# Kernel tuning notes

Measured on AMD Instinct MI355X. Metric: run time of the kernel, lower is better.

Reference implementation:

```python
import jax, jax.numpy as jnp
import numpy as np

B, T, C, H = 4, 4096, 1024, 64

def setup_inputs() -> dict:
    key = jax.random.key(0)
    kx, kq, kk, kv = jax.random.split(key, 4)
    x = jax.random.normal(kx, (B, T, C), dtype=jnp.float32)
    Wq = jax.random.normal(kq, (C, H), dtype=jnp.float32) * (C ** -0.5)
    Wk = jax.random.normal(kk, (C, H), dtype=jnp.float32) * (C ** -0.5)
    Wv = jax.random.normal(kv, (C, H), dtype=jnp.float32) * (C ** -0.5)
    return {"x": x, "Wq": Wq, "Wk": Wk, "Wv": Wv}

def reference(x, Wq, Wk, Wv):
    # single-head causal attention, dropout p=0 (eval)
    q = jnp.einsum('btc,ch->bth', x, Wq)  # [B,T,H]
    k = jnp.einsum('btc,ch->bth', x, Wk)
    v = jnp.einsum('btc,ch->bth', x, Wv)
    scale = k.shape[-1] ** -0.5
    scores = jnp.einsum('bth,bsh->bts', q, k) * scale  # [B,T,T]
    causal = jnp.tril(jnp.ones((q.shape[1], q.shape[1]), dtype=bool))
    scores = jnp.where(causal, scores, -jnp.inf)
    weights = jax.nn.softmax(scores, axis=-1)
    out = jnp.einsum('bts,bsh->bth', weights, v)  # [B,T,H]
    return out
```

## Files before the change

kernel.cpp:

```cpp
#include <hip/hip_runtime.h>


typedef short  s16x8 __attribute__((ext_vector_type(8)));
typedef float  f32x4 __attribute__((ext_vector_type(4)));
typedef unsigned u32x2 __attribute__((ext_vector_type(2)));

constexpr int B = 4, T = 4096, C = 1024, H = 64;
constexpr int M = B * T;
constexpr float LOG2E = 1.44269504088896340736f;
constexpr float QSCALE = 0.125f * LOG2E;
constexpr float MBASE  = 4.0f * LOG2E;

__device__ __forceinline__ unsigned short f2bf(float f) {
    union { float f; unsigned u; } v; v.f = f;
    unsigned r = v.u + 0x7fffu + ((v.u >> 16) & 1u);
    return (unsigned short)(r >> 16);
}

__device__ __forceinline__ unsigned cvt_pk_bf16(float lo, float hi) {
    unsigned r;
    asm("v_cvt_pk_bf16_f32 %0, %1, %2" : "=v"(r) : "v"(lo), "v"(hi));
    return r;
}

__device__ __forceinline__ float vexp2(float x) {
    float r;
    asm("v_exp_f32 %0, %1" : "=v"(r) : "v"(x));
    return r;
}

__device__ __forceinline__ void gl_lds16(const void* g, void* l) {
    __builtin_amdgcn_global_load_lds(
        (const __attribute__((address_space(1))) unsigned*)g,
        (__attribute__((address_space(3))) unsigned*)l, 16, 0, 0);
}

__global__ void prep_w(const float* __restrict__ Wq, const float* __restrict__ Wk,
                       const float* __restrict__ Wv, unsigned short* __restrict__ Wt) {
    const int n = blockIdx.x;
    const float* W = (n < 64) ? Wq : (n < 128 ? Wk : Wv);
    const int col = n & 63;
    for (int k = threadIdx.x; k < C; k += blockDim.x)
        Wt[(size_t)n * C + k] = f2bf(W[(size_t)k * H + col]);
}

__global__ __launch_bounds__(512) void qkv_proj(
    const float* __restrict__ x, const unsigned short* __restrict__ Wt,
    unsigned short* __restrict__ Q, unsigned short* __restrict__ K,
    unsigned short* __restrict__ VT) {
    __shared__ __align__(16) unsigned short ldsA[2][32 * 64];
    __shared__ __align__(16) unsigned short ldsB[2][192 * 64];

    const int t = threadIdx.x, lane = t & 63, w = t >> 6;
    const int i = lane & 15, g = lane >> 4;
    const int rowbase = blockIdx.x * 32;
    const int rw = w & 1, nw = w >> 1;

    const int arow = t >> 3, aslot = t & 7;
    const float* aga = x + (size_t)(rowbase + arow) * C + ((aslot ^ (arow & 7)) * 8);
    const int awoff = arow * 64 + aslot * 8;
    const bool astage = (t < 256);

    const int brow8 = lane >> 3, bslot = lane & 7;
    const unsigned short* bga[3];
    int bn0[3];
#pragma unroll
    for (int j = 0; j < 3; ++j) {
        bn0[j] = w * 24 + j * 8;
        bga[j] = Wt + (size_t)(bn0[j] + brow8) * C + ((bslot ^ brow8) * 8);
    }

    f32x4 acc[3];
#pragma unroll
    for (int n = 0; n < 3; ++n) acc[n] = (f32x4){0.f, 0.f, 0.f, 0.f};

    {
#pragma unroll
        for (int j = 0; j < 3; ++j)
            gl_lds16(bga[j], &ldsB[0][bn0[j] * 64]);
        if (astage) {
            f32x4 a0 = *(const f32x4*)(aga);
            f32x4 a1 = *(const f32x4*)(aga + 4);
            union { unsigned u[4]; s16x8 v; } av;
            av.u[0] = cvt_pk_bf16(a0[0], a0[1]);
            av.u[1] = cvt_pk_bf16(a0[2], a0[3]);
            av.u[2] = cvt_pk_bf16(a1[0], a1[1]);
            av.u[3] = cvt_pk_bf16(a1[2], a1[3]);
            *(s16x8*)&ldsA[0][awoff] = av.v;
        }
    }
    __syncthreads();

    for (int it = 0; it < 16; ++it) {
        const int cur = it & 1, nxt = cur ^ 1;
        const int kc = (it + 1) * 64;
        f32x4 a0, a1;
        const bool more = (it < 15);
        if (more) {
            if (astage) {
                a0 = *(const f32x4*)(aga + kc);
                a1 = *(const f32x4*)(aga + kc + 4);
            }
#pragma unroll
            for (int j = 0; j < 3; ++j)
                gl_lds16(bga[j] + kc, &ldsB[nxt][bn0[j] * 64]);
        }
#pragma unroll
        for (int kst = 0; kst < 2; ++kst) {
            const int c = kst * 4 + g;
            s16x8 a = *(const s16x8*)&ldsA[cur][(rw * 16 + i) * 64 + ((c ^ (i & 7)) * 8)];
#pragma unroll
            for (int nt = 0; nt < 3; ++nt) {
                int n = nw * 48 + nt * 16 + i;
                s16x8 b = *(const s16x8*)&ldsB[cur][n * 64 + ((c ^ (i & 7)) * 8)];
                acc[nt] = __builtin_amdgcn_mfma_f32_16x16x32_bf16(a, b, acc[nt], 0, 0, 0);
            }
        }
        if (more && astage) {
            union { unsigned u[4]; s16x8 v; } av;
            av.u[0] = cvt_pk_bf16(a0[0], a0[1]);
            av.u[1] = cvt_pk_bf16(a0[2], a0[3]);
            av.u[2] = cvt_pk_bf16(a1[0], a1[1]);
            av.u[3] = cvt_pk_bf16(a1[2], a1[3]);
            *(s16x8*)&ldsA[nxt][awoff] = av.v;
        }
        __syncthreads();
    }

#pragma unroll
    for (int nt = 0; nt < 3; ++nt) {
        const int base = nw * 48 + nt * 16;
        const int n = base + i;
        if (base >= 128) {
            const int h = n - 128;
            const int bb = rowbase >> 12, tb = rowbase & 4095;
            u32x2 pk;
            pk[0] = cvt_pk_bf16(acc[nt][0], acc[nt][1]);
            pk[1] = cvt_pk_bf16(acc[nt][2], acc[nt][3]);
            *(u32x2*)(VT + (size_t)(bb * H + h) * T + tb + g * 8 + rw * 4) = pk;
        } else if (base >= 64) {
#pragma unroll
            for (int r = 0; r < 4; ++r)
                K[(size_t)(rowbase + rw * 16 + g * 4 + r) * H + (n - 64)] = f2bf(acc[nt][r]);
        } else {
#pragma unroll
            for (int r = 0; r < 4; ++r)
                Q[(size_t)(rowbase + rw * 16 + g * 4 + r) * H + n] = f2bf(acc[nt][r] * QSCALE);
        }
    }
}

__global__ __launch_bounds__(256) void attn(
    const unsigned short* __restrict__ Qg, const unsigned short* __restrict__ Kg,
    const unsigned short* __restrict__ VTg,
    unsigned short* __restrict__ Opb, float* __restrict__ lpart) {
    __shared__ __align__(16) unsigned short ks[3][64 * 64];
    __shared__ __align__(16) unsigned short vs[3][64 * 64];

    const int t = threadIdx.x, lane = t & 63, w = t >> 6;
    const int bid = blockIdx.x;
    const int b = bid & 3;
    const int sp = (bid >> 2) & 7;
    const int qt = 31 - (bid >> 5);
    const int q0 = qt * 128;
    const int q0w = q0 + w * 32;
    const int i = lane & 15, g = lane >> 4, g4 = g * 4;
    const int nkv = 2 * qt + 2;
    const int nTiles = (sp < nkv) ? ((nkv - sp + 7) >> 3) : 0;

    const unsigned short* Kb = Kg  + (size_t)b * T * H;
    const unsigned short* Vb = VTg + (size_t)b * H * T;

    const int r8 = lane >> 3, sl = lane & 7, sx = sl ^ r8;

    const unsigned short* QrowA = Qg + (size_t)(b * T + q0w + i) * H;
    s16x8 bqa0 = *(const s16x8*)(QrowA + g * 8);
    s16x8 bqa1 = *(const s16x8*)(QrowA + 32 + g * 8);
    const unsigned short* QrowB = QrowA + 16 * H;
    s16x8 bqb0 = *(const s16x8*)(QrowB + g * 8);
    s16x8 bqb1 = *(const s16x8*)(QrowB + 32 + g * 8);

    const f32x4 minit = (f32x4){-MBASE, -MBASE, -MBASE, -MBASE};

    f32x4 oa[4], ob[4];
#pragma unroll
    for (int nt = 0; nt < 4; ++nt) {
        oa[nt] = (f32x4){0.f, 0.f, 0.f, 0.f};
        ob[nt] = (f32x4){0.f, 0.f, 0.f, 0.f};
    }
    float la = 0.f, lb = 0.f;

    if (nTiles > 0) {
        const int kv0 = sp * 64;
#pragma unroll
        for (int j = 0; j < 2; ++j) {
            const int row = (w + j * 4) * 8 + r8;
            gl_lds16(Kb + (size_t)(kv0 + row) * H + sx * 8, &ks[0][row * 64 + sl * 8]);
            gl_lds16(Vb + (size_t)row * T + kv0 + sx * 8,   &vs[0][row * 64 + sl * 8]);
        }
    }
    if (nTiles > 1) {
        const int kv1 = (sp + 8) * 64;
#pragma unroll
        for (int j = 0; j < 2; ++j) {
            const int row = (w + j * 4) * 8 + r8;
            gl_lds16(Kb + (size_t)(kv1 + row) * H + sx * 8, &ks[1][row * 64 + sl * 8]);
            gl_lds16(Vb + (size_t)row * T + kv1 + sx * 8,   &vs[1][row * 64 + sl * 8]);
        }
        asm volatile("s_waitcnt vmcnt(4)\n\ts_barrier" ::: "memory");
    } else {
        asm volatile("s_waitcnt vmcnt(0)\n\ts_barrier" ::: "memory");
    }

    for (int n = 0; n < nTiles; ++n) {
        const int tile = sp + n * 8;
        const int kv = tile * 64;
        const int cur = n % 3;
        const bool issue = (n + 2 < nTiles);

        if (issue) {
            const int nxt = (n + 2) % 3;
            const int kvn = kv + 1024;
#pragma unroll
            for (int j = 0; j < 2; ++j) {
                const int row = (w + j * 4) * 8 + r8;
                gl_lds16(Kb + (size_t)(kvn + row) * H + sx * 8, &ks[nxt][row * 64 + sl * 8]);
                gl_lds16(Vb + (size_t)row * T + kvn + sx * 8,   &vs[nxt][row * 64 + sl * 8]);
            }
        }

        if (kv <= q0w + 31) {
            s16x8 kb[8];
#pragma unroll
            for (int kst = 0; kst < 2; ++kst)
#pragma unroll
                for (int nt = 0; nt < 4; ++nt)
                    kb[kst * 4 + nt] = *(const s16x8*)
                        &ks[cur][(nt * 16 + i) * 64 + (((kst * 4 + g) ^ (i & 7)) * 8)];

            unsigned pa[8], pb2[8];

            {
                f32x4 s[4];
#pragma unroll
                for (int nt = 0; nt < 4; ++nt) {
                    s[nt] = __builtin_amdgcn_mfma_f32_16x16x32_bf16(kb[nt], bqa0, minit, 0, 0, 0);
                    s[nt] = __builtin_amdgcn_mfma_f32_16x16x32_bf16(kb[4 + nt], bqa1, s[nt], 0, 0, 0);
                }
                if (kv + 63 > q0w) {
                    const int thr = q0w + i - kv;
#pragma unroll
                    for (int nt = 0; nt < 4; ++nt)
#pragma unroll
                        for (int r = 0; r < 4; ++r)
                            if (nt * 16 + g4 + r > thr) s[nt][r] = -INFINITY;
                }
#pragma unroll
                for (int nt = 0; nt < 4; ++nt)
#pragma unroll
                    for (int r = 0; r < 4; ++r)
                        s[nt][r] = vexp2(s[nt][r]);
#pragma unroll
                for (int nt = 0; nt < 4; ++nt) {
                    pa[nt * 2]     = cvt_pk_bf16(s[nt][0], s[nt][1]);
                    pa[nt * 2 + 1] = cvt_pk_bf16(s[nt][2], s[nt][3]);
                }
                la += ((s[0][0] + s[0][1]) + (s[0][2] + s[0][3]))
                    + ((s[1][0] + s[1][1]) + (s[1][2] + s[1][3]))
                    + ((s[2][0] + s[2][1]) + (s[2][2] + s[2][3]))
                    + ((s[3][0] + s[3][1]) + (s[3][2] + s[3][3]));
            }

            {
                f32x4 s[4];
#pragma unroll
                for (int nt = 0; nt < 4; ++nt) {
                    s[nt] = __builtin_amdgcn_mfma_f32_16x16x32_bf16(kb[nt], bqb0, minit, 0, 0, 0);
                    s[nt] = __builtin_amdgcn_mfma_f32_16x16x32_bf16(kb[4 + nt], bqb1, s[nt], 0, 0, 0);
                }
                if (kv + 63 > q0w + 16) {
                    const int thr = q0w + 16 + i - kv;
#pragma unroll
                    for (int nt = 0; nt < 4; ++nt)
#pragma unroll
                        for (int r = 0; r < 4; ++r)
                            if (nt * 16 + g4 + r > thr) s[nt][r] = -INFINITY;
                }
#pragma unroll
                for (int nt = 0; nt < 4; ++nt)
#pragma unroll
                    for (int r = 0; r < 4; ++r)
                        s[nt][r] = vexp2(s[nt][r]);
#pragma unroll
                for (int nt = 0; nt < 4; ++nt) {
                    pb2[nt * 2]     = cvt_pk_bf16(s[nt][0], s[nt][1]);
                    pb2[nt * 2 + 1] = cvt_pk_bf16(s[nt][2], s[nt][3]);
                }
                lb += ((s[0][0] + s[0][1]) + (s[0][2] + s[0][3]))
                    + ((s[1][0] + s[1][1]) + (s[1][2] + s[1][3]))
                    + ((s[2][0] + s[2][1]) + (s[2][2] + s[2][3]))
                    + ((s[3][0] + s[3][1]) + (s[3][2] + s[3][3]));
            }

            s16x8 vb[8];
#pragma unroll
            for (int kst = 0; kst < 2; ++kst)
#pragma unroll
                for (int nt = 0; nt < 4; ++nt)
                    vb[kst * 4 + nt] = *(const s16x8*)
                        &vs[cur][(nt * 16 + i) * 64 + (((kst * 4 + g) ^ (i & 7)) * 8)];

#pragma unroll
            for (int kst = 0; kst < 2; ++kst) {
                union { unsigned u[4]; s16x8 v; } fa, fb;
                fa.u[0] = pa[4 * kst];      fa.u[1] = pa[4 * kst + 1];
                fa.u[2] = pa[4 * kst + 2];  fa.u[3] = pa[4 * kst + 3];
                fb.u[0] = pb2[4 * kst];     fb.u[1] = pb2[4 * kst + 1];
                fb.u[2] = pb2[4 * kst + 2]; fb.u[3] = pb2[4 * kst + 3];
#pragma unroll
                for (int nt = 0; nt < 4; ++nt) {
                    oa[nt] = __builtin_amdgcn_mfma_f32_16x16x32_bf16(vb[kst * 4 + nt], fa.v, oa[nt], 0, 0, 0);
                    ob[nt] = __builtin_amdgcn_mfma_f32_16x16x32_bf16(vb[kst * 4 + nt], fb.v, ob[nt], 0, 0, 0);
                }
            }
        }

        if (issue) asm volatile("s_waitcnt vmcnt(4)\n\ts_barrier" ::: "memory");
        else       asm volatile("s_waitcnt vmcnt(0)\n\ts_barrier" ::: "memory");
    }

    la += __shfl_xor(la, 16);  la += __shfl_xor(la, 32);
    lb += __shfl_xor(lb, 16);  lb += __shfl_xor(lb, 32);
    unsigned short* opA = Opb + ((size_t)bid * 128 + w * 32 + i) * 64;
    unsigned short* opB = opA + 16 * 64;
#pragma unroll
    for (int nt = 0; nt < 4; ++nt) {
        u32x2 pk;
        pk[0] = cvt_pk_bf16(oa[nt][0], oa[nt][1]);
        pk[1] = cvt_pk_bf16(oa[nt][2], oa[nt][3]);
        *(u32x2*)(opA + nt * 16 + g4) = pk;
        pk[0] = cvt_pk_bf16(ob[nt][0], ob[nt][1]);
        pk[1] = cvt_pk_bf16(ob[nt][2], ob[nt][3]);
        *(u32x2*)(opB + nt * 16 + g4) = pk;
    }
    if (g == 0) {
        lpart[(size_t)bid * 128 + w * 32 + i]      = la;
        lpart[(size_t)bid * 128 + w * 32 + 16 + i] = lb;
    }
}

__global__ __launch_bounds__(256) void merge8(
    const unsigned short* __restrict__ Opb, const float* __restrict__ lpart,
    float* __restrict__ out) {
    const int idx = blockIdx.x * 256 + threadIdx.x;
    const int row = idx >> 4, c4 = (idx & 15) * 4;
    const int b = row >> 12, q = row & 4095;
    const int qt = q >> 7, r = q & 127;
    const int qti = 31 - qt;

    float L = 0.f;
    f32x4 o = (f32x4){0.f, 0.f, 0.f, 0.f};
#pragma unroll
    for (int sp = 0; sp < 8; ++sp) {
        const int bidp = qti * 32 + sp * 4 + b;
        L += lpart[(size_t)bidp * 128 + r];
        union { unsigned long long d; unsigned short s[4]; } v;
        v.d = *(const unsigned long long*)&Opb[((size_t)bidp * 128 + r) * 64 + c4];
#pragma unroll
        for (int k = 0; k < 4; ++k) {
            union { unsigned u; float f; } cv;
            cv.u = (unsigned)v.s[k] << 16;
            o[k] += cv.f;
        }
    }
    const float inv = 1.0f / L;
    f32x4 res = (f32x4){o[0] * inv, o[1] * inv, o[2] * inv, o[3] * inv};
    *(f32x4*)&out[(size_t)row * 64 + c4] = res;
}

extern "C" void kernel_launch(void* const* d_in, const int* in_sizes, int n_in,
                              void* d_out, int out_size, void* d_ws, size_t ws_size,
                              hipStream_t stream) {
    (void)in_sizes; (void)n_in; (void)out_size; (void)ws_size;
    const float* x  = (const float*)d_in[0];
    const float* Wq = (const float*)d_in[1];
    const float* Wk = (const float*)d_in[2];
    const float* Wv = (const float*)d_in[3];
    float* out = (float*)d_out;

    char* ws = (char*)d_ws;
    unsigned short* Q  = (unsigned short*)(ws);
    unsigned short* K  = (unsigned short*)(ws + (size_t)1 * M * H * 2);
    unsigned short* VT = (unsigned short*)(ws + (size_t)3 * M * H * 2);
    unsigned short* Wt = (unsigned short*)(ws + (size_t)4 * M * H * 2);
    unsigned short* Opb = (unsigned short*)(ws + (size_t)4 * M * H * 2 + 512 * 1024);
    float* lpart = (float*)(ws + (size_t)4 * M * H * 2 + 512 * 1024
                            + (size_t)1024 * 128 * 64 * 2);

    prep_w<<<192, 256, 0, stream>>>(Wq, Wk, Wv, Wt);
    qkv_proj<<<M / 32, 512, 0, stream>>>(x, Wt, Q, K, VT);
    attn<<<1024, 256, 0, stream>>>(Q, K, VT, Opb, lpart);
    merge8<<<1024, 256, 0, stream>>>(Opb, lpart, out);
}
```

Baseline: 50.77 us.

## Compute softmax row sums via MFMA with ones and unroll triple-buffer loop

Replaces the per-lane VALU summation of exponentiated scores and the cross-lane shuffles with an extra MFMA against a vector of bf16 ones, so the row sum comes out of the matrix unit from the same bf16 probabilities used for PV. The tile loop is also unrolled by three with a templated body, making the LDS buffer index a compile-time constant instead of n%3. This trades VALU adds for extra MFMA issue slots and bigger code. The row sum now uses bf16-rounded probabilities, which is arguably more consistent with the numerator.

```diff
diff --git a/kernel.cpp b/kernel.cpp
--- a/kernel.cpp
+++ b/kernel.cpp
@@ -150,6 +150,123 @@
     }
 }
 
+template<int CUR>
+__device__ __forceinline__ void attn_tile(
+    int n, int nTiles, int sp, int q0w, int i, int g, int g4, int w,
+    int r8, int sl, int sx,
+    const unsigned short* Kb, const unsigned short* Vb,
+    unsigned short (&ks)[3][64 * 64], unsigned short (&vs)[3][64 * 64],
+    const s16x8& bqa0, const s16x8& bqa1, const s16x8& bqb0, const s16x8& bqb1,
+    const s16x8& ones, const f32x4& minit,
+    f32x4 (&oa)[4], f32x4 (&ob)[4], f32x4& al, f32x4& bl) {
+    constexpr int NXT = (CUR + 2) % 3;
+    const int kv = (sp + n * 8) * 64;
+    const bool issue = (n + 2 < nTiles);
+
+    if (issue) {
+        const int kvn = kv + 1024;
+#pragma unroll
+        for (int j = 0; j < 2; ++j) {
+            const int row = (w + j * 4) * 8 + r8;
+            gl_lds16(Kb + (size_t)(kvn + row) * H + sx * 8, &ks[NXT][row * 64 + sl * 8]);
+            gl_lds16(Vb + (size_t)row * T + kvn + sx * 8,   &vs[NXT][row * 64 + sl * 8]);
+        }
+    }
+
+    if (kv <= q0w + 31) {
+        s16x8 kb[8];
+#pragma unroll
+        for (int kst = 0; kst < 2; ++kst)
+#pragma unroll
+            for (int nt = 0; nt < 4; ++nt)
+                kb[kst * 4 + nt] = *(const s16x8*)
+                    &ks[CUR][(nt * 16 + i) * 64 + (((kst * 4 + g) ^ (i & 7)) * 8)];
+
+        unsigned pa[8], pb2[8];
+
+        {
+            f32x4 s[4];
+#pragma unroll
+            for (int nt = 0; nt < 4; ++nt) {
+                s[nt] = __builtin_amdgcn_mfma_f32_16x16x32_bf16(kb[nt], bqa0, minit, 0, 0, 0);
+                s[nt] = __builtin_amdgcn_mfma_f32_16x16x32_bf16(kb[4 + nt], bqa1, s[nt], 0, 0, 0);
+            }
+            if (kv + 63 > q0w) {
+                const int thr = q0w + i - kv;
+#pragma unroll
+                for (int nt = 0; nt < 4; ++nt)
+#pragma unroll
+                    for (int r = 0; r < 4; ++r)
+                        if (nt * 16 + g4 + r > thr) s[nt][r] = -INFINITY;
+            }
+#pragma unroll
+            for (int nt = 0; nt < 4; ++nt)
+#pragma unroll
+                for (int r = 0; r < 4; ++r)
+                    s[nt][r] = vexp2(s[nt][r]);
+#pragma unroll
+            for (int nt = 0; nt < 4; ++nt) {
+                pa[nt * 2]     = cvt_pk_bf16(s[nt][0], s[nt][1]);
+                pa[nt * 2 + 1] = cvt_pk_bf16(s[nt][2], s[nt][3]);
+            }
+        }
+
+        {
+            f32x4 s[4];
+#pragma unroll
+            for (int nt = 0; nt < 4; ++nt) {
+                s[nt] = __builtin_amdgcn_mfma_f32_16x16x32_bf16(kb[nt], bqb0, minit, 0, 0, 0);
+                s[nt] = __builtin_amdgcn_mfma_f32_16x16x32_bf16(kb[4 + nt], bqb1, s[nt], 0, 0, 0);
+            }
+            if (kv + 63 > q0w + 16) {
+                const int thr = q0w + 16 + i - kv;
+#pragma unroll
+                for (int nt = 0; nt < 4; ++nt)
+#pragma unroll
+                    for (int r = 0; r < 4; ++r)
+                        if (nt * 16 + g4 + r > thr) s[nt][r] = -INFINITY;
+            }
+#pragma unroll
+            for (int nt = 0; nt < 4; ++nt)
+#pragma unroll
+                for (int r = 0; r < 4; ++r)
+                    s[nt][r] = vexp2(s[nt][r]);
+#pragma unroll
+            for (int nt = 0; nt < 4; ++nt) {
+                pb2[nt * 2]     = cvt_pk_bf16(s[nt][0], s[nt][1]);
+                pb2[nt * 2 + 1] = cvt_pk_bf16(s[nt][2], s[nt][3]);
+            }
+        }
+
+        s16x8 vb[8];
+#pragma unroll
+        for (int kst = 0; kst < 2; ++kst)
+#pragma unroll
+            for (int nt = 0; nt < 4; ++nt)
+                vb[kst * 4 + nt] = *(const s16x8*)
+                    &vs[CUR][(nt * 16 + i) * 64 + (((kst * 4 + g) ^ (i & 7)) * 8)];
+
+#pragma unroll
+        for (int kst = 0; kst < 2; ++kst) {
+            union { unsigned u[4]; s16x8 v; } fa, fb;
+            fa.u[0] = pa[4 * kst];      fa.u[1] = pa[4 * kst + 1];
+            fa.u[2] = pa[4 * kst + 2];  fa.u[3] = pa[4 * kst + 3];
+            fb.u[0] = pb2[4 * kst];     fb.u[1] = pb2[4 * kst + 1];
+            fb.u[2] = pb2[4 * kst + 2]; fb.u[3] = pb2[4 * kst + 3];
+#pragma unroll
+            for (int nt = 0; nt < 4; ++nt) {
+                oa[nt] = __builtin_amdgcn_mfma_f32_16x16x32_bf16(vb[kst * 4 + nt], fa.v, oa[nt], 0, 0, 0);
+                ob[nt] = __builtin_amdgcn_mfma_f32_16x16x32_bf16(vb[kst * 4 + nt], fb.v, ob[nt], 0, 0, 0);
+            }
+            al = __builtin_amdgcn_mfma_f32_16x16x32_bf16(ones, fa.v, al, 0, 0, 0);
+            bl = __builtin_amdgcn_mfma_f32_16x16x32_bf16(ones, fb.v, bl, 0, 0, 0);
+        }
+    }
+
+    if (issue) asm volatile("s_waitcnt vmcnt(4)\n\ts_barrier" ::: "memory");
+    else       asm volatile("s_waitcnt vmcnt(0)\n\ts_barrier" ::: "memory");
+}
+
 __global__ __launch_bounds__(256) void attn(
     const unsigned short* __restrict__ Qg, const unsigned short* __restrict__ Kg,
     const unsigned short* __restrict__ VTg,
@@ -181,6 +298,9 @@
     s16x8 bqb1 = *(const s16x8*)(QrowB + 32 + g * 8);
 
     const f32x4 minit = (f32x4){-MBASE, -MBASE, -MBASE, -MBASE};
+    s16x8 ones;
+#pragma unroll
+    for (int j = 0; j < 8; ++j) ones[j] = (short)0x3F80;
 
     f32x4 oa[4], ob[4];
 #pragma unroll
@@ -188,7 +308,8 @@
         oa[nt] = (f32x4){0.f, 0.f, 0.f, 0.f};
         ob[nt] = (f32x4){0.f, 0.f, 0.f, 0.f};
     }
-    float la = 0.f, lb = 0.f;
+    f32x4 al = (f32x4){0.f, 0.f, 0.f, 0.f};
+    f32x4 bl = (f32x4){0.f, 0.f, 0.f, 0.f};
 
     if (nTiles > 0) {
         const int kv0 = sp * 64;
@@ -212,125 +333,21 @@
         asm volatile("s_waitcnt vmcnt(0)\n\ts_barrier" ::: "memory");
     }
 
-    for (int n = 0; n < nTiles; ++n) {
-        const int tile = sp + n * 8;
-        const int kv = tile * 64;
-        const int cur = n % 3;
-        const bool issue = (n + 2 < nTiles);
-
-        if (issue) {
-            const int nxt = (n + 2) % 3;
-            const int kvn = kv + 1024;
-#pragma unroll
-            for (int j = 0; j < 2; ++j) {
-                const int row = (w + j * 4) * 8 + r8;
-                gl_lds16(Kb + (size_t)(kvn + row) * H + sx * 8, &ks[nxt][row * 64 + sl * 8]);
-                gl_lds16(Vb + (size_t)row * T + kvn + sx * 8,   &vs[nxt][row * 64 + sl * 8]);
-            }
-        }
-
-        if (kv <= q0w + 31) {
-            s16x8 kb[8];
-#pragma unroll
-            for (int kst = 0; kst < 2; ++kst)
-#pragma unroll
-                for (int nt = 0; nt < 4; ++nt)
-                    kb[kst * 4 + nt] = *(const s16x8*)
-                        &ks[cur][(nt * 16 + i) * 64 + (((kst * 4 + g) ^ (i & 7)) * 8)];
-
-            unsigned pa[8], pb2[8];
-
-            {
-                f32x4 s[4];
-#pragma unroll
-                for (int nt = 0; nt < 4; ++nt) {
-                    s[nt] = __builtin_amdgcn_mfma_f32_16x16x32_bf16(kb[nt], bqa0, minit, 0, 0, 0);
-                    s[nt] = __builtin_amdgcn_mfma_f32_16x16x32_bf16(kb[4 + nt], bqa1, s[nt], 0, 0, 0);
-                }
-                if (kv + 63 > q0w) {
-                    const int thr = q0w + i - kv;
-#pragma unroll
-                    for (int nt = 0; nt < 4; ++nt)
-#pragma unroll
-                        for (int r = 0; r < 4; ++r)
-                            if (nt * 16 + g4 + r > thr) s[nt][r] = -INFINITY;
-                }
-#pragma unroll
-                for (int nt = 0; nt < 4; ++nt)
-#pragma unroll
-                    for (int r = 0; r < 4; ++r)
-                        s[nt][r] = vexp2(s[nt][r]);
-#pragma unroll
-                for (int nt = 0; nt < 4; ++nt) {
-                    pa[nt * 2]     = cvt_pk_bf16(s[nt][0], s[nt][1]);
-                    pa[nt * 2 + 1] = cvt_pk_bf16(s[nt][2], s[nt][3]);
-                }
-                la += ((s[0][0] + s[0][1]) + (s[0][2] + s[0][3]))
-                    + ((s[1][0] + s[1][1]) + (s[1][2] + s[1][3]))
-                    + ((s[2][0] + s[2][1]) + (s[2][2] + s[2][3]))
-                    + ((s[3][0] + s[3][1]) + (s[3][2] + s[3][3]));
-            }
-
-            {
-                f32x4 s[4];
-#pragma unroll
-                for (int nt = 0; nt < 4; ++nt) {
-                    s[nt] = __builtin_amdgcn_mfma_f32_16x16x32_bf16(kb[nt], bqb0, minit, 0, 0, 0);
-                    s[nt] = __builtin_amdgcn_mfma_f32_16x16x32_bf16(kb[4 + nt], bqb1, s[nt], 0, 0, 0);
-                }
-                if (kv + 63 > q0w + 16) {
-                    const int thr = q0w + 16 + i - kv;
-#pragma unroll
-                    for (int nt = 0; nt < 4; ++nt)
-#pragma unroll
-                        for (int r = 0; r < 4; ++r)
-                            if (nt * 16 + g4 + r > thr) s[nt][r] = -INFINITY;
-                }
-#pragma unroll
-                for (int nt = 0; nt < 4; ++nt)
-#pragma unroll
-                    for (int r = 0; r < 4; ++r)
-                        s[nt][r] = vexp2(s[nt][r]);
-#pragma unroll
-                for (int nt = 0; nt < 4; ++nt) {
-                    pb2[nt * 2]     = cvt_pk_bf16(s[nt][0], s[nt][1]);
-                    pb2[nt * 2 + 1] = cvt_pk_bf16(s[nt][2], s[nt][3]);
-                }
-                lb += ((s[0][0] + s[0][1]) + (s[0][2] + s[0][3]))
-                    + ((s[1][0] + s[1][1]) + (s[1][2] + s[1][3]))
-                    + ((s[2][0] + s[2][1]) + (s[2][2] + s[2][3]))
-                    + ((s[3][0] + s[3][1]) + (s[3][2] + s[3][3]));
-            }
-
-            s16x8 vb[8];
-#pragma unroll
-            for (int kst = 0; kst < 2; ++kst)
-#pragma unroll
-                for (int nt = 0; nt < 4; ++nt)
-                    vb[kst * 4 + nt] = *(const s16x8*)
-                        &vs[cur][(nt * 16 + i) * 64 + (((kst * 4 + g) ^ (i & 7)) * 8)];
-
-#pragma unroll
-            for (int kst = 0; kst < 2; ++kst) {
-                union { unsigned u[4]; s16x8 v; } fa, fb;
-                fa.u[0] = pa[4 * kst];      fa.u[1] = pa[4 * kst + 1];
-                fa.u[2] = pa[4 * kst + 2];  fa.u[3] = pa[4 * kst + 3];
-                fb.u[0] = pb2[4 * kst];     fb.u[1] = pb2[4 * kst + 1];
-                fb.u[2] = pb2[4 * kst + 2]; fb.u[3] = pb2[4 * kst + 3];
-#pragma unroll
-                for (int nt = 0; nt < 4; ++nt) {
-                    oa[nt] = __builtin_amdgcn_mfma_f32_16x16x32_bf16(vb[kst * 4 + nt], fa.v, oa[nt], 0, 0, 0);
-                    ob[nt] = __builtin_amdgcn_mfma_f32_16x16x32_bf16(vb[kst * 4 + nt], fb.v, ob[nt], 0, 0, 0);
-                }
-            }
-        }
-
-        if (issue) asm volatile("s_waitcnt vmcnt(4)\n\ts_barrier" ::: "memory");
-        else       asm volatile("s_waitcnt vmcnt(0)\n\ts_barrier" ::: "memory");
-    }
-
-    la += __shfl_xor(la, 16);  la += __shfl_xor(la, 32);
-    lb += __shfl_xor(lb, 16);  lb += __shfl_xor(lb, 32);
+    {
+        int n = 0;
+        while (n < nTiles) {
+            attn_tile<0>(n, nTiles, sp, q0w, i, g, g4, w, r8, sl, sx, Kb, Vb,
+                         ks, vs, bqa0, bqa1, bqb0, bqb1, ones, minit, oa, ob, al, bl);
+            if (++n >= nTiles) break;
+            attn_tile<1>(n, nTiles, sp, q0w, i, g, g4, w, r8, sl, sx, Kb, Vb,
+                         ks, vs, bqa0, bqa1, bqb0, bqb1, ones, minit, oa, ob, al, bl);
+            if (++n >= nTiles) break;
+            attn_tile<2>(n, nTiles, sp, q0w, i, g, g4, w, r8, sl, sx, Kb, Vb,
+                         ks, vs, bqa0, bqa1, bqb0, bqb1, ones, minit, oa, ob, al, bl);
+            ++n;
+        }
+    }
+
     unsigned short* opA = Opb + ((size_t)bid * 128 + w * 32 + i) * 64;
     unsigned short* opB = opA + 16 * 64;
 #pragma unroll
@@ -344,8 +361,8 @@
         *(u32x2*)(opB + nt * 16 + g4) = pk;
     }
     if (g == 0) {
-        lpart[(size_t)bid * 128 + w * 32 + i]      = la;
-        lpart[(size_t)bid * 128 + w * 32 + 16 + i] = lb;
+        lpart[(size_t)bid * 128 + w * 32 + i]      = al[0];
+        lpart[(size_t)bid * 128 + w * 32 + 16 + i] = bl[0];
     }
 }
 
```

Result: no change. 50.27 us (-1.0%).
